# Optimization experiments

Measured on AMD Instinct MI355X. Metric: run time of the kernel, lower is better.

## Reference

```python
import jax, jax.numpy as jnp
import numpy as np

D_MODEL, D_STATE, EXPAND, D_CONV, HEADDIM = 1024, 128, 2, 4, 64
D_INNER = EXPAND * D_MODEL                      # 2048
NHEADS = D_INNER // HEADDIM                     # 32
NGROUPS = 1
CONV_DIM = D_INNER + 2 * NGROUPS * D_STATE      # 2304
D_IN_PROJ = 2 * D_INNER + 2 * NGROUPS * D_STATE + NHEADS  # 4384
BATCH, SEQ = 2, 4096
EPS = 1e-5


def setup_inputs() -> dict:
    key = jax.random.key(0)
    ks = jax.random.split(key, 6)
    sn = lambda k, shape, sc: jax.random.normal(k, shape, jnp.float32) * sc
    # dt_bias such that softplus(dt_bias) spans [1e-3, 0.1] (mamba2 init)
    dt = jnp.linspace(1e-3, 0.1, NHEADS)
    return {
        "x": sn(ks[0], (BATCH, SEQ, D_MODEL), 1.0),
        "ln_w": jnp.ones((D_MODEL,), jnp.float32),
        "ln_b": jnp.zeros((D_MODEL,), jnp.float32),
        "in_proj_w": sn(ks[1], (D_IN_PROJ, D_MODEL), D_MODEL ** -0.5),
        "conv_w": sn(ks[2], (CONV_DIM, D_CONV), D_CONV ** -0.5),
        "conv_b": jnp.zeros((CONV_DIM,), jnp.float32),
        "dt_bias": jnp.log(jnp.expm1(dt)).astype(jnp.float32),
        "A_log": jnp.log(jnp.arange(1, NHEADS + 1, dtype=jnp.float32)),
        "D": jnp.ones((NHEADS,), jnp.float32),
        "norm_w": jnp.ones((D_INNER,), jnp.float32),
        "out_proj_w": sn(ks[3], (D_MODEL, D_INNER), D_INNER ** -0.5),
    }


def _mamba2(u, in_proj_w, conv_w, conv_b, dt_bias, A_log, Dp, norm_w, out_proj_w):
    b, l, _ = u.shape
    zxbcdt = u @ in_proj_w.T                              # [b,l,4384]
    z, xBC, dt = jnp.split(zxbcdt, [D_INNER, D_INNER + CONV_DIM], axis=-1)
    # causal depthwise conv1d over channels, then SiLU
    xBC = jnp.transpose(xBC, (0, 2, 1))                   # [b,conv_dim,l]
    xBC = jax.lax.conv_general_dilated(
        xBC, conv_w[:, None, :], window_strides=(1,),
        padding=[(D_CONV - 1, 0)], feature_group_count=CONV_DIM,
        dimension_numbers=("NCH", "OIH", "NCH"))
    xBC = jax.nn.silu(jnp.transpose(xBC, (0, 2, 1)) + conv_b)
    x, Bm, Cm = jnp.split(xBC, [D_INNER, D_INNER + NGROUPS * D_STATE], axis=-1)
    dt = jax.nn.softplus(dt + dt_bias)                    # [b,l,h]
    A = -jnp.exp(A_log)                                   # [h]
    xh = x.reshape(b, l, NHEADS, HEADDIM)
    # time-major for the selective scan
    dt_t, x_t = jnp.moveaxis(dt, 1, 0), jnp.moveaxis(xh, 1, 0)
    B_t, C_t = jnp.moveaxis(Bm, 1, 0), jnp.moveaxis(Cm, 1, 0)

    def step(h, inputs):
        dtk, xk, Bk, Ck = inputs                          # [b,h],[b,h,p],[b,n],[b,n]
        decay = jnp.exp(dtk * A)                          # [b,h]
        h = h * decay[:, :, None, None] + (dtk[:, :, None, None] * xk[..., None]) * Bk[:, None, None, :]
        y = jnp.einsum("bhpn,bn->bhp", h, Ck)
        return h, y

    h0 = jnp.zeros((b, NHEADS, HEADDIM, D_STATE), u.dtype)
    _, ys = jax.lax.scan(step, h0, (dt_t, x_t, B_t, C_t))  # ys: [l,b,h,p]
    y = jnp.moveaxis(ys, 0, 1) + Dp[None, None, :, None] * xh
    y = y.reshape(b, l, D_INNER)
    # gated RMSNorm: rmsnorm(y * silu(z)) * norm_w
    y = y * jax.nn.silu(z)
    y = y * jax.lax.rsqrt(jnp.mean(y * y, axis=-1, keepdims=True) + EPS) * norm_w
    return y @ out_proj_w.T


def reference(x, ln_w, ln_b, in_proj_w, conv_w, conv_b, dt_bias, A_log, D, norm_w, out_proj_w):
    mu = jnp.mean(x, -1, keepdims=True)
    var = jnp.mean((x - mu) ** 2, -1, keepdims=True)
    xn = (x - mu) * jax.lax.rsqrt(var + EPS) * ln_w + ln_b
    # dropout is identity at inference
    return x + _mamba2(xn, in_proj_w, conv_w, conv_b, dt_bias, A_log, D, norm_w, out_proj_w)
```

## Files before the change

kernel.cpp:

```cpp
#include <hip/hip_runtime.h>
#include <cstdint>

#define D_MODEL 1024
#define D_INNER 2048
#define NHEADS 32
#define HEADDIM 64
#define D_STATE 128
#define CONV_DIM 2304
#define D_IN_PROJ 4384
#define SEQ 4096
#define NROWS 8192
#define NPROJ_PAD 4480
#define TCH 128
#define NCHUNK 32
#define CR 8

typedef float f32x4 __attribute__((ext_vector_type(4)));
typedef __bf16 bf16x8 __attribute__((ext_vector_type(8)));
typedef unsigned short u16;

__device__ __forceinline__ u16 f2bf(float f) {
  uint32_t u = __builtin_bit_cast(uint32_t, f);
  u += 0x7FFFu + ((u >> 16) & 1u);
  return (u16)(u >> 16);
}
__device__ __forceinline__ float bf2f(u16 h) {
  return __builtin_bit_cast(float, (uint32_t)h << 16);
}
__device__ __forceinline__ float dexp(float a) { return expf(fminf(0.f, a)); }
__device__ __forceinline__ int sw(int v) { return (((v & 7) ^ ((v >> 3) & 7)) << 3); }

typedef __attribute__((address_space(1))) const void gv_t;
typedef __attribute__((address_space(3))) void lv_t;
__device__ __forceinline__ void gload_lds16(const void* g, void* l) {
  __builtin_amdgcn_global_load_lds((gv_t*)g, (lv_t*)l, 16, 0, 0);
}

__global__ __launch_bounds__(256) void cvt_pad(const float* __restrict__ s,
                                               u16* __restrict__ d, int n_src, int n_dst) {
  int i = (blockIdx.x * 256 + threadIdx.x) * 4;
  int stride = gridDim.x * 256 * 4;
  for (; i < n_dst; i += stride) {
    ushort4 o;
    if (i < n_src) {
      float4 v = *(const float4*)&s[i];
      o.x = f2bf(v.x); o.y = f2bf(v.y); o.z = f2bf(v.z); o.w = f2bf(v.w);
    } else {
      o.x = o.y = o.z = o.w = 0;
    }
    *(ushort4*)&d[i] = o;
  }
}

__global__ __launch_bounds__(256) void cvt_w2s(const float* __restrict__ s,
                                               const float* __restrict__ nw,
                                               u16* __restrict__ d, int n) {
  int i = (blockIdx.x * 256 + threadIdx.x) * 4;
  int stride = gridDim.x * 256 * 4;
  for (; i < n; i += stride) {
    float4 v = *(const float4*)&s[i];
    int c = i & (D_INNER - 1);
    ushort4 o;
    o.x = f2bf(v.x * nw[c]);
    o.y = f2bf(v.y * nw[c + 1]);
    o.z = f2bf(v.z * nw[c + 2]);
    o.w = f2bf(v.w * nw[c + 3]);
    *(ushort4*)&d[i] = o;
  }
}

__global__ __launch_bounds__(256) void ln_kernel(const float* __restrict__ x,
                                                 const float* __restrict__ w,
                                                 const float* __restrict__ b,
                                                 u16* __restrict__ out) {
  int row = blockIdx.x, tid = threadIdx.x;
  const float4 v = *(const float4*)&x[(long)row * D_MODEL + tid * 4];
  float s1 = v.x + v.y + v.z + v.w;
  float s2 = v.x * v.x + v.y * v.y + v.z * v.z + v.w * v.w;
#pragma unroll
  for (int m = 32; m >= 1; m >>= 1) {
    s1 += __shfl_xor(s1, m);
    s2 += __shfl_xor(s2, m);
  }
  __shared__ float p1[4], p2[4];
  if ((tid & 63) == 0) { p1[tid >> 6] = s1; p2[tid >> 6] = s2; }
  __syncthreads();
  s1 = p1[0] + p1[1] + p1[2] + p1[3];
  s2 = p2[0] + p2[1] + p2[2] + p2[3];
  float mean = s1 * (1.f / D_MODEL);
  float var = s2 * (1.f / D_MODEL) - mean * mean;
  float rstd = rsqrtf(var + 1e-5f);
  const float4 wv = *(const float4*)&w[tid * 4];
  const float4 bv = *(const float4*)&b[tid * 4];
  ushort4 o;
  o.x = f2bf((v.x - mean) * rstd * wv.x + bv.x);
  o.y = f2bf((v.y - mean) * rstd * wv.y + bv.y);
  o.z = f2bf((v.z - mean) * rstd * wv.z + bv.z);
  o.w = f2bf((v.w - mean) * rstd * wv.w + bv.w);
  *(ushort4*)&out[(long)row * D_MODEL + tid * 4] = o;
}

template <int MODE>
__global__ __launch_bounds__(256, 4) void gemm_bt(const u16* __restrict__ A,
                                                  const u16* __restrict__ B, int K,
                                                  u16* __restrict__ zb,
                                                  u16* __restrict__ xb,
                                                  float* __restrict__ dtb,
                                                  float* __restrict__ C,
                                                  const float* __restrict__ resid,
                                                  const float* __restrict__ rvec) {
  __shared__ __align__(16) u16 As[128 * 64];
  __shared__ __align__(16) u16 Bs[128 * 64];
  const int tid = threadIdx.x;
  int m0, n0;
  if (MODE == 0) {
    const int k = (blockIdx.x & 7) * 280 + (blockIdx.x >> 3);
    const int st = k / 40, inner = k % 40;
    m0 = ((st & 7) * 8 + (inner & 7)) * 128;
    n0 = ((st >> 3) * 5 + (inner >> 3)) * 128;
  } else {
    const int wg = (blockIdx.x & 7) * 64 + (blockIdx.x >> 3);
    m0 = (wg & 63) * 128;
    n0 = (wg >> 6) * 128;
  }
  const int w = tid >> 6, l = tid & 63;
  const int wm = w >> 1, wn = w & 1;

  f32x4 acc[4][4] = {};

  for (int k0 = 0; k0 < K; k0 += 64) {
#pragma unroll
    for (int i = 0; i < 4; ++i) {
      int idx = i * 256 + tid;
      int row = idx >> 3, slot = idx & 7;
      int ks = slot ^ (row & 7);
      const u16* ga = A + (long)(m0 + row) * K + k0 + ks * 8;
      gload_lds16(ga, (char*)As + idx * 16);
      const u16* gb = B + (long)(n0 + row) * K + k0 + ks * 8;
      gload_lds16(gb, (char*)Bs + idx * 16);
    }
    __syncthreads();
    bf16x8 af[2][4], bfr[2][4];
#pragma unroll
    for (int kk = 0; kk < 2; ++kk)
#pragma unroll
      for (int f = 0; f < 4; ++f) {
        int rowa = wm * 64 + f * 16 + (l & 15);
        int ca = ((kk << 2) | (l >> 4)) ^ (rowa & 7);
        af[kk][f] = *(const bf16x8*)((const char*)As + rowa * 128 + ca * 16);
        int rowb = wn * 64 + f * 16 + (l & 15);
        int cb2 = ((kk << 2) | (l >> 4)) ^ (rowb & 7);
        bfr[kk][f] = *(const bf16x8*)((const char*)Bs + rowb * 128 + cb2 * 16);
      }
#pragma unroll
    for (int kk = 0; kk < 2; ++kk)
#pragma unroll
      for (int mf = 0; mf < 4; ++mf)
#pragma unroll
        for (int nf = 0; nf < 4; ++nf)
          acc[mf][nf] = __builtin_amdgcn_mfma_f32_16x16x32_bf16(
              af[kk][mf], bfr[kk][nf], acc[mf][nf], 0, 0, 0);
    __syncthreads();
  }
#pragma unroll
  for (int mf = 0; mf < 4; ++mf)
#pragma unroll
    for (int nf = 0; nf < 4; ++nf) {
      int col = n0 + wn * 64 + nf * 16 + (l & 15);
#pragma unroll
      for (int r = 0; r < 4; ++r) {
        int rowm = m0 + wm * 64 + mf * 16 + (l >> 4) * 4 + r;
        float v = acc[mf][nf][r];
        if (MODE == 0) {
          if (col < D_INNER)
            zb[(long)rowm * D_INNER + col] = f2bf(v);
          else if (col < D_INNER + CONV_DIM)
            xb[(long)rowm * CONV_DIM + (col - D_INNER)] = f2bf(v);
          else if (col < D_IN_PROJ)
            dtb[(long)rowm * NHEADS + (col - D_INNER - CONV_DIM)] = v;
        } else {
          long off = (long)rowm * D_MODEL + col;
          C[off] = v * rvec[rowm] + resid[off];
        }
      }
    }
}

__global__ __launch_bounds__(256) void conv_silu_kernel(const u16* __restrict__ xr,
                                                        const float* __restrict__ cw,
                                                        const float* __restrict__ cb,
                                                        u16* __restrict__ xp,
                                                        u16* __restrict__ bc) {
  const int c = blockIdx.x * 256 + threadIdx.x;
  const int row0 = blockIdx.y * CR;
  const int t0 = row0 & (SEQ - 1);
  const float4 wv = *(const float4*)&cw[c * 4];
  const float bias = cb[c];
  float xwin[CR + 3];
#pragma unroll
  for (int k = 0; k < CR + 3; ++k) {
    int t = t0 - 3 + k;
    xwin[k] = (t >= 0) ? bf2f(xr[(long)(row0 - 3 + k) * CONV_DIM + c]) : 0.f;
  }
#pragma unroll
  for (int j = 0; j < CR; ++j) {
    float a = bias + xwin[j] * wv.x + xwin[j + 1] * wv.y + xwin[j + 2] * wv.z +
              xwin[j + 3] * wv.w;
    a = a / (1.f + expf(-a));
    int row = row0 + j;
    if (c < D_INNER)
      xp[(long)row * D_INNER + c] = f2bf(a);
    else
      bc[(long)row * (2 * D_STATE) + (c - D_INNER)] = f2bf(a);
  }
}

__global__ __launch_bounds__(256, 3) void ssd_state_kernel(
    const u16* __restrict__ xp, const u16* __restrict__ bcb,
    const float* __restrict__ dtf, const float* __restrict__ dt_bias,
    const float* __restrict__ A_log, u16* __restrict__ S,
    float* __restrict__ cdk) {
  const int hh = blockIdx.x, cc = blockIdx.y, bb = blockIdx.z;
  const int tid = threadIdx.x, w = tid >> 6, l = tid & 63;
  __shared__ __align__(16) u16 BT[128 * 128];
  __shared__ __align__(16) u16 WXT[64 * 128];
  __shared__ float ws[128];
  const long rowbase = (long)bb * SEQ + cc * TCH;
  const float Ah = -expf(A_log[hh]);
  const float dbias = dt_bias[hh];

#pragma unroll
  for (int i = 0; i < 8; ++i) {
    int slot = i * 256 + tid, t = slot >> 4, nb = slot & 15;
    bf16x8 v = *(const bf16x8*)&bcb[(rowbase + t) * 256 + nb * 8];
    const u16* e = (const u16*)&v;
#pragma unroll
    for (int j = 0; j < 8; ++j) {
      int n = nb * 8 + j;
      BT[n * 128 + (t ^ sw(n))] = e[j];
    }
  }
  if (w == 0) {
    float r0 = dtf[(rowbase + l) * NHEADS + hh] + dbias;
    float r1 = dtf[(rowbase + 64 + l) * NHEADS + hh] + dbias;
    float d0 = r0 > 20.f ? r0 : log1pf(expf(r0));
    float d1 = r1 > 20.f ? r1 : log1pf(expf(r1));
    float a0 = d0 * Ah, a1 = d1 * Ah;
#pragma unroll
    for (int d = 1; d < 64; d <<= 1) { float u = __shfl_up(a0, d); if (l >= d) a0 += u; }
#pragma unroll
    for (int d = 1; d < 64; d <<= 1) { float u = __shfl_up(a1, d); if (l >= d) a1 += u; }
    float t0 = __shfl(a0, 63);
    float tot = __shfl(a1, 63) + t0;
    ws[l] = dexp(tot - a0) * d0;
    ws[64 + l] = dexp(tot - (a1 + t0)) * d1;
    if (l == 0) cdk[(bb * 32 + hh) * NCHUNK + cc] = dexp(tot);
  }
  __syncthreads();
#pragma unroll
  for (int i = 0; i < 4; ++i) {
    int slot = i * 256 + tid, t = slot >> 3, pb = slot & 7;
    bf16x8 v = *(const bf16x8*)&xp[(rowbase + t) * D_INNER + hh * 64 + pb * 8];
    float wt = ws[t];
    const u16* e = (const u16*)&v;
#pragma unroll
    for (int j = 0; j < 8; ++j) {
      int p = pb * 8 + j;
      WXT[p * 128 + (t ^ sw(p))] = f2bf(bf2f(e[j]) * wt);
    }
  }
  __syncthreads();

  f32x4 acc[8] = {};
  const int p = w * 16 + (l & 15);
  const int swp = sw(p);
#pragma unroll
  for (int kc = 0; kc < 4; ++kc) {
    int tsl = kc * 32 + (l >> 4) * 8;
    bf16x8 af = *(const bf16x8*)&WXT[p * 128 + (tsl ^ swp)];
#pragma unroll
    for (int nt = 0; nt < 8; ++nt) {
      int n = nt * 16 + (l & 15);
      bf16x8 bfv = *(const bf16x8*)&BT[n * 128 + (tsl ^ sw(n))];
      acc[nt] = __builtin_amdgcn_mfma_f32_16x16x32_bf16(af, bfv, acc[nt], 0, 0, 0);
    }
  }
  u16* Sb = S + ((long)(bb * 32 + hh) * NCHUNK + cc) * 8192;
#pragma unroll
  for (int nt = 0; nt < 8; ++nt)
#pragma unroll
    for (int r = 0; r < 4; ++r) {
      int prow = w * 16 + (l >> 4) * 4 + r;
      Sb[prow * 128 + nt * 16 + (l & 15)] = f2bf(acc[nt][r]);
    }
}

__global__ __launch_bounds__(256) void ssd_combine(u16* __restrict__ SH,
                                                   const float* __restrict__ cdk) {
  const int hh = blockIdx.y, bb = blockIdx.z;
  const int pp = blockIdx.x * 16 + (threadIdx.x >> 4);
  const int nn = (threadIdx.x & 15) * 8;
  const int bh = bb * 32 + hh;
  u16* base = SH + (long)bh * NCHUNK * 8192 + pp * 128 + nn;
  const float* ck = cdk + bh * NCHUNK;
  float h[8] = {};
  for (int c = 0; c < NCHUNK; ++c) {
    bf16x8 sv = *(bf16x8*)(base + (long)c * 8192);
    const u16* se = (const u16*)&sv;
    u16 o[8];
#pragma unroll
    for (int j = 0; j < 8; ++j) o[j] = f2bf(h[j]);
    *(bf16x8*)(base + (long)c * 8192) = *(bf16x8*)o;
    float d = ck[c];
#pragma unroll
    for (int j = 0; j < 8; ++j) h[j] = fmaf(h[j], d, bf2f(se[j]));
  }
}

__global__ __launch_bounds__(256, 3) void ssd_y_kernel(
    const u16* __restrict__ xp, const u16* __restrict__ bcb,
    const float* __restrict__ dtf, const float* __restrict__ dt_bias,
    const float* __restrict__ A_log, const float* __restrict__ Dp,
    const u16* __restrict__ H, u16* __restrict__ zb,
    float* __restrict__ psum) {
  const int hh = blockIdx.x, cc = blockIdx.y, bb = blockIdx.z;
  const int tid = threadIdx.x, w = tid >> 6, l = tid & 63;
  __shared__ __align__(16) u16 XT[64 * 128];
  __shared__ __align__(16) u16 Ms[128 * 136];
  __shared__ float sig[128], dts[128], esg[128];
  const long rowbase = (long)bb * SEQ + cc * TCH;
  const float Ah = -expf(A_log[hh]);
  const float Dh = Dp[hh];
  const float dbias = dt_bias[hh];

  if (w == 0) {
    float r0 = dtf[(rowbase + l) * NHEADS + hh] + dbias;
    float r1 = dtf[(rowbase + 64 + l) * NHEADS + hh] + dbias;
    float d0 = r0 > 20.f ? r0 : log1pf(expf(r0));
    float d1 = r1 > 20.f ? r1 : log1pf(expf(r1));
    float a0 = d0 * Ah, a1 = d1 * Ah;
#pragma unroll
    for (int d = 1; d < 64; d <<= 1) { float u = __shfl_up(a0, d); if (l >= d) a0 += u; }
#pragma unroll
    for (int d = 1; d < 64; d <<= 1) { float u = __shfl_up(a1, d); if (l >= d) a1 += u; }
    float t0 = __shfl(a0, 63);
    sig[l] = a0; sig[64 + l] = a1 + t0;
    dts[l] = d0; dts[64 + l] = d1;
    esg[l] = dexp(a0); esg[64 + l] = dexp(a1 + t0);
  }
#pragma unroll
  for (int i = 0; i < 4; ++i) {
    int slot = i * 256 + tid, t = slot >> 3, pb = slot & 7;
    bf16x8 v = *(const bf16x8*)&xp[(rowbase + t) * D_INNER + hh * 64 + pb * 8];
    const u16* e = (const u16*)&v;
#pragma unroll
    for (int j = 0; j < 8; ++j) {
      int p = pb * 8 + j;
      XT[p * 128 + (t ^ sw(p))] = e[j];
    }
  }
  __syncthreads();

  bf16x8 cfr[2][4];
#pragma unroll
  for (int tt = 0; tt < 2; ++tt) {
    int t = (w * 2 + tt) * 16 + (l & 15);
#pragma unroll
    for (int kc = 0; kc < 4; ++kc)
      cfr[tt][kc] = *(const bf16x8*)&bcb[(rowbase + t) * 256 + 128 + kc * 32 +
                                         (l >> 4) * 8];
  }
  f32x4 g[2][8] = {};
#pragma unroll
  for (int st = 0; st < 8; ++st) {
    int s = st * 16 + (l & 15);
#pragma unroll
    for (int kc = 0; kc < 4; ++kc) {
      bf16x8 bfv = *(const bf16x8*)&bcb[(rowbase + s) * 256 + kc * 32 + (l >> 4) * 8];
      g[0][st] = __builtin_amdgcn_mfma_f32_16x16x32_bf16(cfr[0][kc], bfv, g[0][st], 0, 0, 0);
      g[1][st] = __builtin_amdgcn_mfma_f32_16x16x32_bf16(cfr[1][kc], bfv, g[1][st], 0, 0, 0);
    }
  }
#pragma unroll
  for (int tt = 0; tt < 2; ++tt)
#pragma unroll
    for (int st = 0; st < 8; ++st)
#pragma unroll
      for (int r = 0; r < 4; ++r) {
        int t = (w * 2 + tt) * 16 + (l >> 4) * 4 + r;
        int s = st * 16 + (l & 15);
        float m = 0.f;
        if (s <= t) m = g[tt][st][r] * dexp(sig[t] - sig[s]) * dts[s];
        Ms[t * 136 + s] = f2bf(m);
      }
  __syncthreads();

  f32x4 y1[2][4] = {};
#pragma unroll
  for (int kc = 0; kc < 4; ++kc) {
    int t0r = (w * 2) * 16 + (l & 15);
    int t1r = (w * 2 + 1) * 16 + (l & 15);
    bf16x8 mf0 = *(const bf16x8*)&Ms[t0r * 136 + kc * 32 + (l >> 4) * 8];
    bf16x8 mf1 = *(const bf16x8*)&Ms[t1r * 136 + kc * 32 + (l >> 4) * 8];
#pragma unroll
    for (int pt = 0; pt < 4; ++pt) {
      int p = pt * 16 + (l & 15);
      int ssl = kc * 32 + (l >> 4) * 8;
      bf16x8 xf = *(const bf16x8*)&XT[p * 128 + (ssl ^ sw(p))];
      y1[0][pt] = __builtin_amdgcn_mfma_f32_16x16x32_bf16(mf0, xf, y1[0][pt], 0, 0, 0);
      y1[1][pt] = __builtin_amdgcn_mfma_f32_16x16x32_bf16(mf1, xf, y1[1][pt], 0, 0, 0);
    }
  }
  f32x4 y2[2][4] = {};
  const u16* Hb = H + ((long)(bb * 32 + hh) * NCHUNK + cc) * 8192;
#pragma unroll
  for (int pt = 0; pt < 4; ++pt) {
    int p = pt * 16 + (l & 15);
#pragma unroll
    for (int kc = 0; kc < 4; ++kc) {
      bf16x8 hf = *(const bf16x8*)&Hb[p * 128 + kc * 32 + (l >> 4) * 8];
      y2[0][pt] = __builtin_amdgcn_mfma_f32_16x16x32_bf16(cfr[0][kc], hf, y2[0][pt], 0, 0, 0);
      y2[1][pt] = __builtin_amdgcn_mfma_f32_16x16x32_bf16(cfr[1][kc], hf, y2[1][pt], 0, 0, 0);
    }
  }
  float s2[2][4] = {};
#pragma unroll
  for (int tt = 0; tt < 2; ++tt)
#pragma unroll
    for (int pt = 0; pt < 4; ++pt)
#pragma unroll
      for (int r = 0; r < 4; ++r) {
        int t = (w * 2 + tt) * 16 + (l >> 4) * 4 + r;
        int p = pt * 16 + (l & 15);
        float xv = bf2f(XT[p * 128 + (t ^ sw(p))]);
        float yv = y1[tt][pt][r] + esg[t] * y2[tt][pt][r] + Dh * xv;
        long off = (rowbase + t) * (long)D_INNER + hh * 64 + p;
        float zv = bf2f(zb[off]);
        float gg = yv * (zv / (1.f + expf(-zv)));
        zb[off] = f2bf(gg);
        s2[tt][r] += gg * gg;
      }
#pragma unroll
  for (int tt = 0; tt < 2; ++tt)
#pragma unroll
    for (int r = 0; r < 4; ++r) {
      float v = s2[tt][r];
      v += __shfl_xor(v, 1);
      v += __shfl_xor(v, 2);
      v += __shfl_xor(v, 4);
      v += __shfl_xor(v, 8);
      if ((l & 15) == 0) {
        int t = (w * 2 + tt) * 16 + (l >> 4) * 4 + r;
        psum[(rowbase + t) * NHEADS + hh] = v;
      }
    }
}

__global__ __launch_bounds__(256) void r_reduce(const float* __restrict__ psum,
                                                float* __restrict__ rvec) {
  int row = blockIdx.x * 256 + threadIdx.x;
  const float4* p = (const float4*)&psum[(long)row * NHEADS];
  float s = 0.f;
#pragma unroll
  for (int i = 0; i < 8; ++i) {
    float4 v = p[i];
    s += v.x + v.y + v.z + v.w;
  }
  rvec[row] = rsqrtf(s * (1.f / D_INNER) + 1e-5f);
}

extern "C" void kernel_launch(void* const* d_in, const int* in_sizes, int n_in,
                              void* d_out, int out_size, void* d_ws, size_t ws_size,
                              hipStream_t stream) {
  const float* x = (const float*)d_in[0];
  const float* ln_w = (const float*)d_in[1];
  const float* ln_b = (const float*)d_in[2];
  const float* in_proj_w = (const float*)d_in[3];
  const float* conv_w = (const float*)d_in[4];
  const float* conv_b = (const float*)d_in[5];
  const float* dt_bias = (const float*)d_in[6];
  const float* A_log = (const float*)d_in[7];
  const float* Dvec = (const float*)d_in[8];
  const float* norm_w = (const float*)d_in[9];
  const float* out_proj_w = (const float*)d_in[10];
  float* out = (float*)d_out;

  char* ws = (char*)d_ws;
  u16* W2bf = (u16*)(ws + 0);
  u16* zbf = (u16*)(ws + 4194304);
  u16* xpart = (u16*)(ws + 37748736);
  u16* bcbf = (u16*)(ws + 71303168);
  float* dtf = (float*)(ws + 75497472);
  float* cdk = (float*)(ws + 76546048);
  u16* W1bf = (u16*)(ws + 76554240);
  u16* xbcraw = (u16*)(ws + 85729280);
  u16* SH = (u16*)(ws + 76554240);
  float* psum = (float*)(ws + 110108672);
  float* rvec = (float*)(ws + 111157248);
  u16* xnbf = (u16*)d_out;

  cvt_pad<<<512, 256, 0, stream>>>(in_proj_w, W1bf, D_IN_PROJ * D_MODEL,
                                   NPROJ_PAD * D_MODEL);
  cvt_w2s<<<512, 256, 0, stream>>>(out_proj_w, norm_w, W2bf, D_MODEL * D_INNER);
  ln_kernel<<<NROWS, 256, 0, stream>>>(x, ln_w, ln_b, xnbf);
  gemm_bt<0><<<35 * 64, 256, 0, stream>>>(xnbf, W1bf, D_MODEL, zbf, xbcraw, dtf,
                                          nullptr, nullptr, nullptr);
  conv_silu_kernel<<<dim3(9, NROWS / CR), 256, 0, stream>>>(xbcraw, conv_w, conv_b,
                                                            xpart, bcbf);
  ssd_state_kernel<<<dim3(32, NCHUNK, 2), 256, 0, stream>>>(xpart, bcbf, dtf, dt_bias,
                                                            A_log, SH, cdk);
  ssd_combine<<<dim3(4, 32, 2), 256, 0, stream>>>(SH, cdk);
  ssd_y_kernel<<<dim3(32, NCHUNK, 2), 256, 0, stream>>>(xpart, bcbf, dtf, dt_bias,
                                                        A_log, Dvec, SH, zbf, psum);
  r_reduce<<<32, 256, 0, stream>>>(psum, rvec);
  gemm_bt<1><<<8 * 64, 256, 0, stream>>>(zbf, W2bf, D_INNER, nullptr, nullptr,
                                         nullptr, out, x, rvec);
}
```

Measured before the change: 301.2 us.

## Hoist head-independent C·Bᵀ Gram matrix and dt cumsum out of SSD y kernel

Since NGROUPS=1, the C·Bᵀ chunk Gram matrix is the same for every head. It is now computed once per (batch, chunk) in a new kernel and stored to a swizzled global buffer, instead of being recomputed by each of the 32 head blocks. A separate small kernel precomputes the softplus dt, the cumulative log-decay and its exponential per chunk/head. The y kernel loads G into LDS via direct global-to-LDS loads, applies the causal decay mask in place, and reuses that buffer for the MFMA. This cuts redundant MFMA work at the cost of two extra launches and extra global traffic for G and the dt buffers.

Measured after the change: 285.0 us. 5.4% less time.

```diff
diff --git a/kernel.cpp b/kernel.cpp
--- a/kernel.cpp
+++ b/kernel.cpp
@@ -215,6 +215,73 @@
   }
 }
 
+__global__ __launch_bounds__(64) void dt_pre(const float* __restrict__ dtf,
+                                             const float* __restrict__ dt_bias,
+                                             const float* __restrict__ A_log,
+                                             float* __restrict__ sgb,
+                                             float* __restrict__ dsb,
+                                             float* __restrict__ egb) {
+  const int cc = blockIdx.x, hh = blockIdx.y, bb = blockIdx.z;
+  const int l = threadIdx.x;
+  const float Ah = -expf(A_log[hh]);
+  const float dbias = dt_bias[hh];
+  const long rowbase = (long)bb * SEQ + cc * TCH;
+  float r0 = dtf[(rowbase + l) * NHEADS + hh] + dbias;
+  float r1 = dtf[(rowbase + 64 + l) * NHEADS + hh] + dbias;
+  float d0 = r0 > 20.f ? r0 : log1pf(expf(r0));
+  float d1 = r1 > 20.f ? r1 : log1pf(expf(r1));
+  float a0 = d0 * Ah, a1 = d1 * Ah;
+#pragma unroll
+  for (int d = 1; d < 64; d <<= 1) { float u = __shfl_up(a0, d); if (l >= d) a0 += u; }
+#pragma unroll
+  for (int d = 1; d < 64; d <<= 1) { float u = __shfl_up(a1, d); if (l >= d) a1 += u; }
+  float t0 = __shfl(a0, 63);
+  float s1 = a1 + t0;
+  const long idx = ((long)(bb * 32 + hh) * 32 + cc) * 128;
+  sgb[idx + l] = a0;       sgb[idx + 64 + l] = s1;
+  dsb[idx + l] = d0;       dsb[idx + 64 + l] = d1;
+  egb[idx + l] = dexp(a0); egb[idx + 64 + l] = dexp(s1);
+}
+
+__global__ __launch_bounds__(256, 2) void ssd_g_kernel(const u16* __restrict__ bcb,
+                                                       u16* __restrict__ Gsw) {
+  const int cc = blockIdx.x, bb = blockIdx.y;
+  const int tid = threadIdx.x, w = tid >> 6, l = tid & 63;
+  const long rowbase = (long)bb * SEQ + cc * TCH;
+  bf16x8 cfr[2][4];
+#pragma unroll
+  for (int tt = 0; tt < 2; ++tt) {
+    int t = (w * 2 + tt) * 16 + (l & 15);
+#pragma unroll
+    for (int kc = 0; kc < 4; ++kc)
+      cfr[tt][kc] = *(const bf16x8*)&bcb[(rowbase + t) * 256 + 128 + kc * 32 +
+                                         (l >> 4) * 8];
+  }
+  f32x4 g[2][8] = {};
+#pragma unroll
+  for (int st = 0; st < 8; ++st) {
+    int s = st * 16 + (l & 15);
+#pragma unroll
+    for (int kc = 0; kc < 4; ++kc) {
+      bf16x8 bfv = *(const bf16x8*)&bcb[(rowbase + s) * 256 + kc * 32 + (l >> 4) * 8];
+      g[0][st] = __builtin_amdgcn_mfma_f32_16x16x32_bf16(cfr[0][kc], bfv, g[0][st], 0, 0, 0);
+      g[1][st] = __builtin_amdgcn_mfma_f32_16x16x32_bf16(cfr[1][kc], bfv, g[1][st], 0, 0, 0);
+    }
+  }
+  u16* Gb = Gsw + (long)(bb * 32 + cc) * 16384;
+#pragma unroll
+  for (int tt = 0; tt < 2; ++tt)
+#pragma unroll
+    for (int st = 0; st < 8; ++st)
+#pragma unroll
+      for (int r = 0; r < 4; ++r) {
+        int t = (w * 2 + tt) * 16 + (l >> 4) * 4 + r;
+        int s = st * 16 + (l & 15);
+        int j = ((((s >> 3) ^ (t & 15)) << 3) | (s & 7));
+        Gb[t * 128 + j] = f2bf(g[tt][st][r]);
+      }
+}
+
 __global__ __launch_bounds__(256, 3) void ssd_state_kernel(
     const u16* __restrict__ xp, const u16* __restrict__ bcb,
     const float* __restrict__ dtf, const float* __restrict__ dt_bias,
@@ -319,34 +386,29 @@
 
 __global__ __launch_bounds__(256, 3) void ssd_y_kernel(
     const u16* __restrict__ xp, const u16* __restrict__ bcb,
-    const float* __restrict__ dtf, const float* __restrict__ dt_bias,
-    const float* __restrict__ A_log, const float* __restrict__ Dp,
-    const u16* __restrict__ H, u16* __restrict__ zb,
-    float* __restrict__ psum) {
+    const u16* __restrict__ Gsw, const float* __restrict__ sgb,
+    const float* __restrict__ dsb, const float* __restrict__ egb,
+    const float* __restrict__ Dp, const u16* __restrict__ H,
+    u16* __restrict__ zb, float* __restrict__ psum) {
   const int hh = blockIdx.x, cc = blockIdx.y, bb = blockIdx.z;
   const int tid = threadIdx.x, w = tid >> 6, l = tid & 63;
+  __shared__ __align__(16) u16 Gs[128 * 128];
   __shared__ __align__(16) u16 XT[64 * 128];
-  __shared__ __align__(16) u16 Ms[128 * 136];
   __shared__ float sig[128], dts[128], esg[128];
   const long rowbase = (long)bb * SEQ + cc * TCH;
-  const float Ah = -expf(A_log[hh]);
   const float Dh = Dp[hh];
-  const float dbias = dt_bias[hh];
-
-  if (w == 0) {
-    float r0 = dtf[(rowbase + l) * NHEADS + hh] + dbias;
-    float r1 = dtf[(rowbase + 64 + l) * NHEADS + hh] + dbias;
-    float d0 = r0 > 20.f ? r0 : log1pf(expf(r0));
-    float d1 = r1 > 20.f ? r1 : log1pf(expf(r1));
-    float a0 = d0 * Ah, a1 = d1 * Ah;
-#pragma unroll
-    for (int d = 1; d < 64; d <<= 1) { float u = __shfl_up(a0, d); if (l >= d) a0 += u; }
-#pragma unroll
-    for (int d = 1; d < 64; d <<= 1) { float u = __shfl_up(a1, d); if (l >= d) a1 += u; }
-    float t0 = __shfl(a0, 63);
-    sig[l] = a0; sig[64 + l] = a1 + t0;
-    dts[l] = d0; dts[64 + l] = d1;
-    esg[l] = dexp(a0); esg[64 + l] = dexp(a1 + t0);
+
+  const u16* Gb = Gsw + (long)(bb * 32 + cc) * 16384;
+#pragma unroll
+  for (int i = 0; i < 8; ++i) {
+    int idx = i * 256 + tid;
+    gload_lds16(Gb + idx * 8, (char*)Gs + idx * 16);
+  }
+  const long sidx = ((long)(bb * 32 + hh) * 32 + cc) * 128;
+  if (tid < 128) {
+    sig[tid] = sgb[sidx + tid];
+    dts[tid] = dsb[sidx + tid];
+    esg[tid] = egb[sidx + tid];
   }
 #pragma unroll
   for (int i = 0; i < 4; ++i) {
@@ -359,8 +421,6 @@
       XT[p * 128 + (t ^ sw(p))] = e[j];
     }
   }
-  __syncthreads();
-
   bf16x8 cfr[2][4];
 #pragma unroll
   for (int tt = 0; tt < 2; ++tt) {
@@ -370,45 +430,46 @@
       cfr[tt][kc] = *(const bf16x8*)&bcb[(rowbase + t) * 256 + 128 + kc * 32 +
                                          (l >> 4) * 8];
   }
-  f32x4 g[2][8] = {};
-#pragma unroll
-  for (int st = 0; st < 8; ++st) {
-    int s = st * 16 + (l & 15);
-#pragma unroll
-    for (int kc = 0; kc < 4; ++kc) {
-      bf16x8 bfv = *(const bf16x8*)&bcb[(rowbase + s) * 256 + kc * 32 + (l >> 4) * 8];
-      g[0][st] = __builtin_amdgcn_mfma_f32_16x16x32_bf16(cfr[0][kc], bfv, g[0][st], 0, 0, 0);
-      g[1][st] = __builtin_amdgcn_mfma_f32_16x16x32_bf16(cfr[1][kc], bfv, g[1][st], 0, 0, 0);
-    }
-  }
-#pragma unroll
-  for (int tt = 0; tt < 2; ++tt)
-#pragma unroll
-    for (int st = 0; st < 8; ++st)
-#pragma unroll
-      for (int r = 0; r < 4; ++r) {
-        int t = (w * 2 + tt) * 16 + (l >> 4) * 4 + r;
-        int s = st * 16 + (l & 15);
+  __syncthreads();
+
+  {
+    const int t = tid >> 1, half = tid & 1;
+    const float sigt = sig[t];
+#pragma unroll
+    for (int wb = 0; wb < 8; ++wb) {
+      int sblkL = half * 8 + wb;
+      int sb2 = sblkL ^ (t & 15);
+      bf16x8 v = *(const bf16x8*)&Gs[t * 128 + sb2 * 8];
+      const u16* ge = (const u16*)&v;
+      u16 o[8];
+#pragma unroll
+      for (int j = 0; j < 8; ++j) {
+        int s = sblkL * 8 + j;
         float m = 0.f;
-        if (s <= t) m = g[tt][st][r] * dexp(sig[t] - sig[s]) * dts[s];
-        Ms[t * 136 + s] = f2bf(m);
-      }
+        if (s <= t) m = bf2f(ge[j]) * dexp(sigt - sig[s]) * dts[s];
+        o[j] = f2bf(m);
+      }
+      *(bf16x8*)&Gs[t * 128 + sb2 * 8] = *(bf16x8*)o;
+    }
+  }
   __syncthreads();
 
   f32x4 y1[2][4] = {};
 #pragma unroll
   for (int kc = 0; kc < 4; ++kc) {
-    int t0r = (w * 2) * 16 + (l & 15);
-    int t1r = (w * 2 + 1) * 16 + (l & 15);
-    bf16x8 mf0 = *(const bf16x8*)&Ms[t0r * 136 + kc * 32 + (l >> 4) * 8];
-    bf16x8 mf1 = *(const bf16x8*)&Ms[t1r * 136 + kc * 32 + (l >> 4) * 8];
-#pragma unroll
-    for (int pt = 0; pt < 4; ++pt) {
-      int p = pt * 16 + (l & 15);
-      int ssl = kc * 32 + (l >> 4) * 8;
-      bf16x8 xf = *(const bf16x8*)&XT[p * 128 + (ssl ^ sw(p))];
-      y1[0][pt] = __builtin_amdgcn_mfma_f32_16x16x32_bf16(mf0, xf, y1[0][pt], 0, 0, 0);
-      y1[1][pt] = __builtin_amdgcn_mfma_f32_16x16x32_bf16(mf1, xf, y1[1][pt], 0, 0, 0);
+#pragma unroll
+    for (int tt = 0; tt < 2; ++tt) {
+      int t = (w * 2 + tt) * 16 + (l & 15);
+      int want = kc * 4 + (l >> 4);
+      int sb2 = want ^ (t & 15);
+      bf16x8 mf = *(const bf16x8*)&Gs[t * 128 + sb2 * 8];
+#pragma unroll
+      for (int pt = 0; pt < 4; ++pt) {
+        int p = pt * 16 + (l & 15);
+        int ssl = kc * 32 + (l >> 4) * 8;
+        bf16x8 xf = *(const bf16x8*)&XT[p * 128 + (ssl ^ sw(p))];
+        y1[tt][pt] = __builtin_amdgcn_mfma_f32_16x16x32_bf16(mf, xf, y1[tt][pt], 0, 0, 0);
+      }
     }
   }
   f32x4 y2[2][4] = {};
@@ -497,6 +558,10 @@
   u16* SH = (u16*)(ws + 76554240);
   float* psum = (float*)(ws + 110108672);
   float* rvec = (float*)(ws + 111157248);
+  u16* Gsw = (u16*)(ws + 111190016);
+  float* sgb = (float*)(ws + 113287168);
+  float* dsb = (float*)(ws + 114335744);
+  float* egb = (float*)(ws + 115384320);
   u16* xnbf = (u16*)d_out;
 
   cvt_pad<<<512, 256, 0, stream>>>(in_proj_w, W1bf, D_IN_PROJ * D_MODEL,
@@ -507,11 +572,14 @@
                                           nullptr, nullptr, nullptr);
   conv_silu_kernel<<<dim3(9, NROWS / CR), 256, 0, stream>>>(xbcraw, conv_w, conv_b,
                                                             xpart, bcbf);
+  dt_pre<<<dim3(NCHUNK, NHEADS, 2), 64, 0, stream>>>(dtf, dt_bias, A_log, sgb, dsb,
+                                                     egb);
+  ssd_g_kernel<<<dim3(NCHUNK, 2), 256, 0, stream>>>(bcbf, Gsw);
   ssd_state_kernel<<<dim3(32, NCHUNK, 2), 256, 0, stream>>>(xpart, bcbf, dtf, dt_bias,
                                                             A_log, SH, cdk);
   ssd_combine<<<dim3(4, 32, 2), 256, 0, stream>>>(SH, cdk);
-  ssd_y_kernel<<<dim3(32, NCHUNK, 2), 256, 0, stream>>>(xpart, bcbf, dtf, dt_bias,
-                                                        A_log, Dvec, SH, zbf, psum);
+  ssd_y_kernel<<<dim3(32, NCHUNK, 2), 256, 0, stream>>>(xpart, bcbf, Gsw, sgb, dsb,
+                                                        egb, Dvec, SH, zbf, psum);
   r_reduce<<<32, 256, 0, stream>>>(psum, rvec);
   gemm_bt<1><<<8 * 64, 256, 0, stream>>>(zbf, W2bf, D_INNER, nullptr, nullptr,
                                          nullptr, out, x, rvec);
```
